# Kernel tuning notes

Measured on AMD Instinct MI355X. Metric: run time of the kernel, lower is better.

Reference implementation:

```python
import jax, jax.numpy as jnp
import numpy as np

M, C, K, D = 2048, 16, 8, 256  # queries, classes, clusters/class, feature_dim
H1, H2 = D, D // 2             # MLP hidden sizes


def setup_inputs() -> dict:
    key = jax.random.key(0)
    ks = jax.random.split(key, 8)
    s1 = 1.0 / np.sqrt(2 * D)
    s2 = 1.0 / np.sqrt(H1)
    s3 = 1.0 / np.sqrt(H2)
    return {
        "query_features": jax.random.normal(ks[0], (M, D), jnp.float32),
        "prototypes": jax.random.normal(ks[1], (C, K, D), jnp.float32),
        "W1": jax.random.normal(ks[2], (2 * D, H1), jnp.float32) * s1,
        "b1": jnp.zeros((H1,), jnp.float32),
        "W2": jax.random.normal(ks[3], (H1, H2), jnp.float32) * s2,
        "b2": jnp.zeros((H2,), jnp.float32),
        "W3": jax.random.normal(ks[4], (H2, 1), jnp.float32) * s3,
        "b3": jnp.zeros((1,), jnp.float32),
    }


def reference(query_features, prototypes, W1, b1, W2, b2, W3, b3):
    # Attention MLP on concat([query, prototype]) for every (query, class, cluster)
    # pair. Split W1 into the query half and prototype half so we never
    # materialize the [M,C,K,2D] concat; broadcast-add instead.
    d = query_features.shape[-1]
    Wq, Wp = W1[:d], W1[d:]
    qh = query_features @ Wq                      # [M, H1]
    ph = jnp.einsum('ckd,dh->ckh', prototypes, Wp)  # [C, K, H1]
    h = jax.nn.relu(qh[:, None, None, :] + ph[None] + b1)   # [M, C, K, H1]
    h = jax.nn.relu(h @ W2 + b2)                              # [M, C, K, H2]
    scores = (h @ W3)[..., 0] + b3[0]                         # [M, C, K]
    attn = jax.nn.softmax(scores, axis=-1)                    # softmax over clusters
    weighted = jnp.einsum('mck,ckd->mcd', attn, prototypes)   # [M, C, D]
    diff = query_features[:, None, :] - weighted              # [M, C, D]
    distances = jnp.sqrt(jnp.sum(diff * diff, axis=-1))       # [M, C]
    return -distances
```

## Files before the change

kernel.cpp:

```cpp
#include <hip/hip_runtime.h>
#include <hip/hip_fp16.h>
#include <cstdint>

typedef __attribute__((ext_vector_type(8))) _Float16 f16x8;
typedef __attribute__((ext_vector_type(4))) float f32x4;
typedef __attribute__((ext_vector_type(16))) float f32x16;

__device__ __forceinline__ f16x8 cvt8(float4 x, float4 y) {
    f16x8 r;
    r[0] = (_Float16)x.x; r[1] = (_Float16)x.y; r[2] = (_Float16)x.z; r[3] = (_Float16)x.w;
    r[4] = (_Float16)y.x; r[5] = (_Float16)y.y; r[6] = (_Float16)y.z; r[7] = (_Float16)y.w;
    return r;
}

__device__ __forceinline__ f16x8 relu8(f16x8 v) {
    f16x8 z = {};
    return __builtin_elementwise_max(v, z);
}

__global__ __launch_bounds__(256, 2)
void prep1(const float* __restrict__ query,
           const float* __restrict__ prot,
           const float* __restrict__ W1,
           const float* __restrict__ b1,
           const float* __restrict__ W2,
           const float* __restrict__ b2,
           _Float16* __restrict__ qh16,
           float* __restrict__ sqp,
           _Float16* __restrict__ phpk,
           f16x8* __restrict__ w2p,
           float* __restrict__ Gm,
           float* __restrict__ q2) {
    __shared__ _Float16 Bls[64][280];
    int b = blockIdx.x, t = threadIdx.x;

    if (b < 200) {
        int mode, row0, col0;
        if (b < 128)      { mode = 0; row0 = (b >> 2) * 64;         col0 = (b & 3) * 64; }
        else if (b < 192) { mode = 1; row0 = ((b - 128) >> 1) * 64; col0 = ((b - 128) & 1) * 64; }
        else              { mode = 2; row0 = ((b - 192) >> 2) * 64; col0 = ((b - 192) & 3) * 64; }
        const float* Asrc = (mode == 2) ? prot : query;

        if (mode != 1) {
            int woff = (mode == 2) ? 256 : 0;
            int rr = t >> 4, c4 = (t & 15) * 4;
            for (int rt = 0; rt < 4; ++rt) {
                #pragma unroll
                for (int it = 0; it < 4; ++it) {
                    int k = rt * 64 + it * 16 + rr;
                    float4 v = *(const float4*)(W1 + (woff + k) * 256 + col0 + c4);
                    Bls[c4 + 0][k] = (_Float16)v.x;
                    Bls[c4 + 1][k] = (_Float16)v.y;
                    Bls[c4 + 2][k] = (_Float16)v.z;
                    Bls[c4 + 3][k] = (_Float16)v.w;
                }
            }
            __syncthreads();
        }

        int w = t >> 6, l = t & 63, l15 = l & 15, l4 = l >> 4;
        f32x4 acc[4];
        #pragma unroll
        for (int nt = 0; nt < 4; ++nt) acc[nt] = (f32x4){0.f, 0.f, 0.f, 0.f};

        for (int ks = 0; ks < 8; ++ks) {
            int row = row0 + w * 16 + l15;
            const float* ap = Asrc + row * 256 + ks * 32 + l4 * 8;
            f16x8 af = cvt8(*(const float4*)ap, *(const float4*)(ap + 4));
            f16x8 bf[4];
            #pragma unroll
            for (int nt = 0; nt < 4; ++nt) {
                if (mode == 1) {
                    int col = col0 + nt * 16 + l15;
                    const float* bp = prot + col * 256 + ks * 32 + l4 * 8;
                    bf[nt] = cvt8(*(const float4*)bp, *(const float4*)(bp + 4));
                } else {
                    bf[nt] = *(const f16x8*)(&Bls[nt * 16 + l15][ks * 32 + l4 * 8]);
                }
            }
            #pragma unroll
            for (int nt = 0; nt < 4; ++nt)
                acc[nt] = __builtin_amdgcn_mfma_f32_16x16x32_f16(af, bf[nt], acc[nt], 0, 0, 0);
        }
        #pragma unroll
        for (int nt = 0; nt < 4; ++nt)
            #pragma unroll
            for (int j = 0; j < 4; ++j) {
                int row = row0 + w * 16 + l4 * 4 + j;
                int col = col0 + nt * 16 + l15;
                float v = acc[nt][j];
                if (mode == 0) {
                    _Float16 v16 = (_Float16)v;
                    __builtin_nontemporal_store(v16, &qh16[row * 256 + col]);
                } else if (mode == 1) {
                    __builtin_nontemporal_store(v, &sqp[row * 128 + col]);
                } else {
                    _Float16 v16 = (_Float16)(v + b1[col]);
                    __builtin_nontemporal_store(v16,
                        &phpk[(((col >> 4) * 2 + ((col >> 3) & 1)) * 128 + row) * 8 + (col & 7)]);
                }
            }
    } else if (b < 217) {
        int chunk = (b - 200) * 256 + t;
        int ks = chunk >> 8, h = (chunk >> 7) & 1, c = chunk & 127;
        f16x8 o = {};
        if (ks < 16) {
            #pragma unroll
            for (int j = 0; j < 8; ++j)
                o[j] = (_Float16)W2[(ks * 16 + h * 8 + j) * 128 + c];
        } else if (h == 0) {
            o[0] = (_Float16)b2[c];
        }
        __builtin_nontemporal_store(o, &w2p[chunk]);
    } else if (b < 249) {
        int pid = (b - 217) * 32 + (t >> 3), l8 = t & 7;
        int c = pid >> 6, k = (pid >> 3) & 7, kp = pid & 7;
        const float4* pa = (const float4*)(prot + (c * 8 + k) * 256 + l8 * 32);
        const float4* pb = (const float4*)(prot + (c * 8 + kp) * 256 + l8 * 32);
        float s = 0.f;
        #pragma unroll
        for (int i = 0; i < 8; ++i) {
            float4 x = pa[i], y = pb[i];
            s += x.x * y.x + x.y * y.y + x.z * y.z + x.w * y.w;
        }
        s += __shfl_xor(s, 1); s += __shfl_xor(s, 2); s += __shfl_xor(s, 4);
        if (l8 == 0) __builtin_nontemporal_store(s, &Gm[pid]);
    } else {
        int m = (b - 249) * 32 + (t >> 3), l8 = t & 7;
        const float4* qp = (const float4*)(query + m * 256 + l8 * 32);
        float s = 0.f;
        #pragma unroll
        for (int i = 0; i < 8; ++i) {
            float4 x = qp[i];
            s += x.x * x.x + x.y * x.y + x.z * x.z + x.w * x.w;
        }
        s += __shfl_xor(s, 1); s += __shfl_xor(s, 2); s += __shfl_xor(s, 4);
        if (l8 == 0) __builtin_nontemporal_store(s, &q2[m]);
    }
}

__global__ __launch_bounds__(256, 1)
void fused6(const _Float16* __restrict__ qh16,
            const uint4* __restrict__ phpk,
            const uint4* __restrict__ w2p,
            const float* __restrict__ sqp,
            const float* __restrict__ q2,
            const float* __restrict__ Gm,
            const float* __restrict__ W3,
            const float* __restrict__ b2,
            float* __restrict__ out) {
    __shared__ _Float16 qlds[16 * 256];
    __shared__ uint4 phl[1024];
    __shared__ float w3l[128];
    __shared__ float b2l[128];
    __shared__ float spart[2][4][4][32];

    int t = threadIdx.x;
    int cs = t >> 6, l = t & 63;
    int lk = l & 31, h = l >> 5;
    int cks = blockIdx.x & 3;
    int mg = blockIdx.x >> 2;
    int m0 = mg * 16;

    const _Float16* w2h = (const _Float16*)w2p;

    ((uint4*)qlds)[t]       = ((const uint4*)(qh16 + m0 * 256))[t];
    ((uint4*)qlds)[t + 256] = ((const uint4*)(qh16 + m0 * 256))[t + 256];
    #pragma unroll
    for (int i = 0; i < 4; ++i) {
        int j = t + i * 256;
        phl[j] = phpk[(j >> 5) * 128 + cks * 32 + (j & 31)];
    }
    if (t < 128) { w3l[t] = W3[t]; b2l[t] = b2[t]; }

    f16x8 wA[16];
    #pragma unroll
    for (int ks = 0; ks < 16; ++ks)
        wA[ks] = *(const f16x8*)(w2h + ((ks * 2 + h) * 128 + cs * 32 + lk) * 8);

    __syncthreads();

    const f16x8* phlh = (const f16x8*)phl;

    for (int pass = 0; pass < 4; ++pass) {
        int mA = m0 + pass * 4;
        const _Float16* qr0 = qlds + (pass * 4 + 0) * 256 + h * 8;
        const _Float16* qr1 = qr0 + 256;
        const _Float16* qr2 = qr0 + 512;
        const _Float16* qr3 = qr0 + 768;

        f32x16 acc0 = {}, acc1 = {}, acc2 = {}, acc3 = {};

        f16x8 qv0[2], qv1[2], qv2[2], qv3[2];
        #pragma unroll
        for (int p = 0; p < 2; ++p) {
            qv0[p] = *(const f16x8*)(qr0 + p * 16);
            qv1[p] = *(const f16x8*)(qr1 + p * 16);
            qv2[p] = *(const f16x8*)(qr2 + p * 16);
            qv3[p] = *(const f16x8*)(qr3 + p * 16);
        }

        #pragma unroll
        for (int ks = 0; ks < 16; ++ks) {
            f16x8 phf = phlh[(ks * 2 + h) * 32 + lk];
            f16x8 a0 = relu8(qv0[ks & 1] + phf);
            f16x8 a1 = relu8(qv1[ks & 1] + phf);
            f16x8 a2 = relu8(qv2[ks & 1] + phf);
            f16x8 a3 = relu8(qv3[ks & 1] + phf);
            if (ks < 14) {
                qv0[ks & 1] = *(const f16x8*)(qr0 + (ks + 2) * 16);
                qv1[ks & 1] = *(const f16x8*)(qr1 + (ks + 2) * 16);
                qv2[ks & 1] = *(const f16x8*)(qr2 + (ks + 2) * 16);
                qv3[ks & 1] = *(const f16x8*)(qr3 + (ks + 2) * 16);
            }
            acc0 = __builtin_amdgcn_mfma_f32_32x32x16_f16(wA[ks], a0, acc0, 0, 0, 0);
            acc1 = __builtin_amdgcn_mfma_f32_32x32x16_f16(wA[ks], a1, acc1, 0, 0, 0);
            acc2 = __builtin_amdgcn_mfma_f32_32x32x16_f16(wA[ks], a2, acc2, 0, 0, 0);
            acc3 = __builtin_amdgcn_mfma_f32_32x32x16_f16(wA[ks], a3, acc3, 0, 0, 0);
        }

        int buf = pass & 1;
        auto score1 = [&](const f32x16& A) -> float {
            float s0 = 0.f, s1 = 0.f, s2 = 0.f, s3 = 0.f;
            #pragma unroll
            for (int r = 0; r < 16; r += 4) {
                int c0i = cs * 32 + ((r + 0) & 3) + 8 * ((r + 0) >> 2) + 4 * h;
                int c1i = cs * 32 + ((r + 1) & 3) + 8 * ((r + 1) >> 2) + 4 * h;
                int c2i = cs * 32 + ((r + 2) & 3) + 8 * ((r + 2) >> 2) + 4 * h;
                int c3i = cs * 32 + ((r + 3) & 3) + 8 * ((r + 3) >> 2) + 4 * h;
                s0 = fmaf(fmaxf(A[r + 0] + b2l[c0i], 0.f), w3l[c0i], s0);
                s1 = fmaf(fmaxf(A[r + 1] + b2l[c1i], 0.f), w3l[c1i], s1);
                s2 = fmaf(fmaxf(A[r + 2] + b2l[c2i], 0.f), w3l[c2i], s2);
                s3 = fmaf(fmaxf(A[r + 3] + b2l[c3i], 0.f), w3l[c3i], s3);
            }
            float s = (s0 + s1) + (s2 + s3);
            s += __shfl_xor(s, 32);
            return s;
        };
        float sc0 = score1(acc0), sc1 = score1(acc1), sc2 = score1(acc2), sc3 = score1(acc3);
        if (l < 32) {
            spart[buf][0][cs][lk] = sc0;
            spart[buf][1][cs][lk] = sc1;
            spart[buf][2][cs][lk] = sc2;
            spart[buf][3][cs][lk] = sc3;
        }
        __syncthreads();

        if (t < 128) {
            int msel = t >> 5, cl = t & 31, kk = t & 7;
            int m = mA + msel;
            int cg = cks * 4 + (cl >> 3);
            float s = spart[buf][msel][0][cl] + spart[buf][msel][1][cl]
                    + spart[buf][msel][2][cl] + spart[buf][msel][3][cl];
            float mx = s;
            mx = fmaxf(mx, __shfl_xor(mx, 1));
            mx = fmaxf(mx, __shfl_xor(mx, 2));
            mx = fmaxf(mx, __shfl_xor(mx, 4));
            float e = __expf(s - mx);
            float den = e;
            den += __shfl_xor(den, 1); den += __shfl_xor(den, 2); den += __shfl_xor(den, 4);
            float a = e / den;
            float p2 = a * __builtin_nontemporal_load(&sqp[m * 128 + cks * 32 + cl]);
            float p3 = 0.f;
            #pragma unroll
            for (int kq = 0; kq < 8; ++kq) {
                float ak = __shfl(a, (l & 56) | kq);
                p3 = fmaf(ak, Gm[cg * 64 + kq * 8 + kk], p3);
            }
            p3 *= a;
            float pr = p3 - 2.f * p2;
            pr += __shfl_xor(pr, 1); pr += __shfl_xor(pr, 2); pr += __shfl_xor(pr, 4);
            if (kk == 0)
                out[m * 16 + cg] = -sqrtf(fmaxf(q2[m] + pr, 0.f));
        }
    }
}

extern "C" void kernel_launch(void* const* d_in, const int* in_sizes, int n_in,
                              void* d_out, int out_size, void* d_ws, size_t ws_size,
                              hipStream_t stream) {
    const float* query = (const float*)d_in[0];
    const float* prot  = (const float*)d_in[1];
    const float* W1    = (const float*)d_in[2];
    const float* b1    = (const float*)d_in[3];
    const float* W2    = (const float*)d_in[4];
    const float* b2    = (const float*)d_in[5];
    const float* W3    = (const float*)d_in[6];

    char* ws = (char*)d_ws;
    _Float16* qh16 = (_Float16*)(ws);
    f16x8*    w2p  = (f16x8*)(ws + 1048576);
    _Float16* phpk = (_Float16*)(ws + 1118208);
    float*    sqp  = (float*)(ws + 1183744);
    float*    q2   = (float*)(ws + 2232320);
    float*    Gm   = (float*)(ws + 2240512);
    float* out = (float*)d_out;

    prep1<<<313, 256, 0, stream>>>(query, prot, W1, b1, W2, b2,
                                   qh16, sqp, phpk, w2p, Gm, q2);
    fused6<<<512, 256, 0, stream>>>(qh16, (const uint4*)phpk, (const uint4*)w2p,
                                    sqp, q2, Gm, W3, b2, out);
}
```

Baseline: 39.69 us.

## Halve queries per block to double grid size and stage epilogue inputs in LDS

Each block now handles 8 queries instead of 16, doing two queries per pass with two MFMA accumulators instead of four, and the grid doubles to 1024 blocks for better CU coverage. The per-block squared-prototype projections, Gram matrix slice and query norms are preloaded into shared memory so the softmax epilogue reads LDS rather than global memory. The trade-off is that the W2 register fragments and prototype tile are reloaded by twice as many blocks, and there is less MFMA work per sync to hide latency.

```diff
diff --git a/kernel.cpp b/kernel.cpp
--- a/kernel.cpp
+++ b/kernel.cpp
@@ -140,7 +140,7 @@
 }
 
 __global__ __launch_bounds__(256, 1)
-void fused6(const _Float16* __restrict__ qh16,
+void fused7(const _Float16* __restrict__ qh16,
             const uint4* __restrict__ phpk,
             const uint4* __restrict__ w2p,
             const float* __restrict__ sqp,
@@ -149,29 +149,37 @@
             const float* __restrict__ W3,
             const float* __restrict__ b2,
             float* __restrict__ out) {
-    __shared__ _Float16 qlds[16 * 256];
+    __shared__ _Float16 qlds[8 * 256];
     __shared__ uint4 phl[1024];
     __shared__ float w3l[128];
     __shared__ float b2l[128];
-    __shared__ float spart[2][4][4][32];
+    __shared__ float sql[8 * 32];
+    __shared__ float gml[256];
+    __shared__ float q2l[8];
+    __shared__ float spart[2][2][4][32];
 
     int t = threadIdx.x;
     int cs = t >> 6, l = t & 63;
     int lk = l & 31, h = l >> 5;
     int cks = blockIdx.x & 3;
     int mg = blockIdx.x >> 2;
-    int m0 = mg * 16;
+    int m0 = mg * 8;
 
     const _Float16* w2h = (const _Float16*)w2p;
 
-    ((uint4*)qlds)[t]       = ((const uint4*)(qh16 + m0 * 256))[t];
-    ((uint4*)qlds)[t + 256] = ((const uint4*)(qh16 + m0 * 256))[t + 256];
+    ((uint4*)qlds)[t] = ((const uint4*)(qh16 + m0 * 256))[t];
     #pragma unroll
     for (int i = 0; i < 4; ++i) {
         int j = t + i * 256;
         phl[j] = phpk[(j >> 5) * 128 + cks * 32 + (j & 31)];
     }
     if (t < 128) { w3l[t] = W3[t]; b2l[t] = b2[t]; }
+    {
+        int rloc = t >> 5, c = t & 31;
+        sql[t] = __builtin_nontemporal_load(&sqp[(m0 + rloc) * 128 + cks * 32 + c]);
+        gml[t] = Gm[cks * 256 + t];
+        if (t < 8) q2l[t] = q2[m0 + t];
+    }
 
     f16x8 wA[16];
     #pragma unroll
@@ -183,21 +191,16 @@
     const f16x8* phlh = (const f16x8*)phl;
 
     for (int pass = 0; pass < 4; ++pass) {
-        int mA = m0 + pass * 4;
-        const _Float16* qr0 = qlds + (pass * 4 + 0) * 256 + h * 8;
+        const _Float16* qr0 = qlds + (pass * 2) * 256 + h * 8;
         const _Float16* qr1 = qr0 + 256;
-        const _Float16* qr2 = qr0 + 512;
-        const _Float16* qr3 = qr0 + 768;
-
-        f32x16 acc0 = {}, acc1 = {}, acc2 = {}, acc3 = {};
-
-        f16x8 qv0[2], qv1[2], qv2[2], qv3[2];
+
+        f32x16 acc0 = {}, acc1 = {};
+
+        f16x8 qv0[2], qv1[2];
         #pragma unroll
         for (int p = 0; p < 2; ++p) {
             qv0[p] = *(const f16x8*)(qr0 + p * 16);
             qv1[p] = *(const f16x8*)(qr1 + p * 16);
-            qv2[p] = *(const f16x8*)(qr2 + p * 16);
-            qv3[p] = *(const f16x8*)(qr3 + p * 16);
         }
 
         #pragma unroll
@@ -205,18 +208,12 @@
             f16x8 phf = phlh[(ks * 2 + h) * 32 + lk];
             f16x8 a0 = relu8(qv0[ks & 1] + phf);
             f16x8 a1 = relu8(qv1[ks & 1] + phf);
-            f16x8 a2 = relu8(qv2[ks & 1] + phf);
-            f16x8 a3 = relu8(qv3[ks & 1] + phf);
             if (ks < 14) {
                 qv0[ks & 1] = *(const f16x8*)(qr0 + (ks + 2) * 16);
                 qv1[ks & 1] = *(const f16x8*)(qr1 + (ks + 2) * 16);
-                qv2[ks & 1] = *(const f16x8*)(qr2 + (ks + 2) * 16);
-                qv3[ks & 1] = *(const f16x8*)(qr3 + (ks + 2) * 16);
             }
             acc0 = __builtin_amdgcn_mfma_f32_32x32x16_f16(wA[ks], a0, acc0, 0, 0, 0);
             acc1 = __builtin_amdgcn_mfma_f32_32x32x16_f16(wA[ks], a1, acc1, 0, 0, 0);
-            acc2 = __builtin_amdgcn_mfma_f32_32x32x16_f16(wA[ks], a2, acc2, 0, 0, 0);
-            acc3 = __builtin_amdgcn_mfma_f32_32x32x16_f16(wA[ks], a3, acc3, 0, 0, 0);
         }
 
         int buf = pass & 1;
@@ -237,19 +234,19 @@
             s += __shfl_xor(s, 32);
             return s;
         };
-        float sc0 = score1(acc0), sc1 = score1(acc1), sc2 = score1(acc2), sc3 = score1(acc3);
+        float sc0 = score1(acc0);
+        float sc1 = score1(acc1);
         if (l < 32) {
             spart[buf][0][cs][lk] = sc0;
             spart[buf][1][cs][lk] = sc1;
-            spart[buf][2][cs][lk] = sc2;
-            spart[buf][3][cs][lk] = sc3;
         }
         __syncthreads();
 
-        if (t < 128) {
+        if (t < 64) {
             int msel = t >> 5, cl = t & 31, kk = t & 7;
-            int m = mA + msel;
-            int cg = cks * 4 + (cl >> 3);
+            int rloc = pass * 2 + msel;
+            int m = m0 + rloc;
+            int cgl = cl >> 3;
             float s = spart[buf][msel][0][cl] + spart[buf][msel][1][cl]
                     + spart[buf][msel][2][cl] + spart[buf][msel][3][cl];
             float mx = s;
@@ -260,18 +257,18 @@
             float den = e;
             den += __shfl_xor(den, 1); den += __shfl_xor(den, 2); den += __shfl_xor(den, 4);
             float a = e / den;
-            float p2 = a * __builtin_nontemporal_load(&sqp[m * 128 + cks * 32 + cl]);
+            float p2 = a * sql[rloc * 32 + cl];
             float p3 = 0.f;
             #pragma unroll
             for (int kq = 0; kq < 8; ++kq) {
                 float ak = __shfl(a, (l & 56) | kq);
-                p3 = fmaf(ak, Gm[cg * 64 + kq * 8 + kk], p3);
+                p3 = fmaf(ak, gml[cgl * 64 + kq * 8 + kk], p3);
             }
             p3 *= a;
             float pr = p3 - 2.f * p2;
             pr += __shfl_xor(pr, 1); pr += __shfl_xor(pr, 2); pr += __shfl_xor(pr, 4);
             if (kk == 0)
-                out[m * 16 + cg] = -sqrtf(fmaxf(q2[m] + pr, 0.f));
+                out[m * 16 + cks * 4 + cgl] = -sqrtf(fmaxf(q2l[rloc] + pr, 0.f));
         }
     }
 }
@@ -298,6 +295,6 @@
 
     prep1<<<313, 256, 0, stream>>>(query, prot, W1, b1, W2, b2,
                                    qh16, sqp, phpk, w2p, Gm, q2);
-    fused6<<<512, 256, 0, stream>>>(qh16, (const uint4*)phpk, (const uint4*)w2p,
-                                    sqp, q2, Gm, W3, b2, out);
-}
+    fused7<<<1024, 256, 0, stream>>>(qh16, (const uint4*)phpk, (const uint4*)w2p,
+                                     sqp, q2, Gm, W3, b2, out);
+}
```

Result: slower. 40.50 us (+2.0%).
